# Performance work log

Measured on AMD Instinct MI355X. Metric: run time of the kernel, lower is better.

Reference implementation:

```python
import jax, jax.numpy as jnp
import numpy as np

B, S, D_IN, D_Q, D_V, H = 2, 2048, 1024, 1024, 1024, 16
HD_Q, HD_V = D_Q // H, D_V // H
SCALE = float(D_Q) ** 0.5  # source scales by sqrt(d_q), NOT sqrt(head_dim)


def setup_inputs() -> dict:
    key = jax.random.key(0)
    k1, k2, k3, k4, k5 = jax.random.split(key, 5)
    return {
        "x": jax.random.normal(k1, (B, S, D_IN), dtype=jnp.float32),
        "w_q": jax.random.normal(k2, (D_IN, D_Q), dtype=jnp.float32),
        "w_k": jax.random.normal(k3, (D_IN, D_Q), dtype=jnp.float32),
        "w_v": jax.random.normal(k4, (D_IN, D_V), dtype=jnp.float32),
        "W_o": jax.random.normal(k5, (D_IN, D_V), dtype=jnp.float32),
    }


def reference(x, w_q, w_k, w_v, W_o):
    b, s, _ = x.shape
    # projections: [b, s, d]
    q = x @ w_q
    k = x @ w_k
    v = x @ w_v
    # split heads -> [b, h, s, hd]
    Q = q.reshape(b, s, H, HD_Q).transpose(0, 2, 1, 3)
    K = k.reshape(b, s, H, HD_Q).transpose(0, 2, 1, 3)
    V = v.reshape(b, s, H, HD_V).transpose(0, 2, 1, 3)
    # full [b, h, s, s] score matrix (naive attention, as in source)
    scores = jnp.einsum("bhqd,bhkd->bhqk", Q, K)
    # FAITHFUL QUIRK: source applies softmax over dim=0 (batch axis)
    attn = jax.nn.softmax(scores / SCALE, axis=0)
    vals = jnp.einsum("bhqk,bhkd->bhqd", attn, V)
    vals = vals.transpose(0, 2, 1, 3).reshape(b, s, D_V)
    return vals @ W_o
```

## Files before the change

kernel.cpp:

```cpp
#include <hip/hip_runtime.h>


typedef _Float16 f16;
typedef __attribute__((ext_vector_type(8))) _Float16 f16x8;
typedef __attribute__((ext_vector_type(4))) _Float16 f16x4;
typedef __attribute__((ext_vector_type(4))) float f32x4;

#define MFMA16(a,b,c) __builtin_amdgcn_mfma_f32_16x16x32_f16(a,b,c,0,0,0)
#define GLD16(gp, lp) __builtin_amdgcn_global_load_lds(                         \
    (const __attribute__((address_space(1))) void*)(gp),                        \
    (__attribute__((address_space(3))) void*)(lp), 16, 0, 0)

__global__ __launch_bounds__(256) void convert_x(const float* __restrict__ x,
                                                 f16* __restrict__ xh, int n4) {
    int i = blockIdx.x * 256 + threadIdx.x;
    if (i >= n4) return;
    float4 v = ((const float4*)x)[i];
    f16x4 h;
    h[0] = (f16)v.x; h[1] = (f16)v.y; h[2] = (f16)v.z; h[3] = (f16)v.w;
    *(f16x4*)(xh + (long)i * 4) = h;
}

__global__ __launch_bounds__(256) void transpose_w(const float* __restrict__ w0, const float* __restrict__ w1,
                                                   const float* __restrict__ w2, const float* __restrict__ w3,
                                                   f16* __restrict__ o0, f16* __restrict__ o1,
                                                   f16* __restrict__ o2, f16* __restrict__ o3) {
    const float* w; f16* o;
    switch (blockIdx.z) {
        case 0: w = w0; o = o0; break;
        case 1: w = w1; o = o1; break;
        case 2: w = w2; o = o2; break;
        default: w = w3; o = o3; break;
    }
    __shared__ alignas(16) f16 t[64][72];
    const int tid = threadIdx.x;
    const int d0 = blockIdx.x * 64, j0 = blockIdx.y * 64;
    #pragma unroll
    for (int it = 0; it < 4; ++it) {
        int idx = it * 256 + tid;
        int row = idx >> 4, c4 = idx & 15;
        float4 v = *(const float4*)(w + (long)(d0 + row) * 1024 + j0 + c4 * 4);
        f16x4 h;
        h[0] = (f16)v.x; h[1] = (f16)v.y; h[2] = (f16)v.z; h[3] = (f16)v.w;
        *(f16x4*)&t[row][c4 * 4] = h;
    }
    __syncthreads();
    #pragma unroll
    for (int it = 0; it < 4; ++it) {
        int idx = it * 256 + tid;
        int jr = idx >> 4, d4 = idx & 15;
        f16x4 h;
        #pragma unroll
        for (int m = 0; m < 4; ++m) h[m] = t[d4 * 4 + m][jr];
        *(f16x4*)(o + (long)(j0 + jr) * 1024 + d0 + d4 * 4) = h;
    }
}

__global__ __launch_bounds__(256, 1) void gemm_qkv(const f16* __restrict__ A,
                                                   const f16* __restrict__ Wt,
                                                   f16* __restrict__ Qg,
                                                   f16* __restrict__ Kg,
                                                   f16* __restrict__ Vtg) {
    __shared__ alignas(16) f16 As[128][64];
    __shared__ alignas(16) f16 Bs[128][64];
    const int tid = threadIdx.x;
    const int wave = tid >> 6, lane = tid & 63;
    const int l15 = lane & 15, lq = lane >> 4;
    const int sw = l15 & 7;
    const int m0 = blockIdx.x * 128, n0 = blockIdx.y * 128;
    const int wr = (wave >> 1) * 64, wc = (wave & 1) * 64;
    const int r8 = lane >> 3;
    const int swc8 = ((lane & 7) ^ r8) * 8;

    f32x4 acc[4][4] = {};

    for (int kt = 0; kt < 16; ++kt) {
        __syncthreads();
        #pragma unroll
        for (int i = 0; i < 4; ++i) {
            GLD16(A  + (long)(m0 + wave * 32 + i * 8 + r8) * 1024 + kt * 64 + swc8, &As[wave * 32 + i * 8][0]);
            GLD16(Wt + (long)(n0 + wave * 32 + i * 8 + r8) * 1024 + kt * 64 + swc8, &Bs[wave * 32 + i * 8][0]);
        }
        __syncthreads();
        #pragma unroll
        for (int s2 = 0; s2 < 2; ++s2) {
            const int rc = ((s2 * 4 + lq) ^ sw) << 3;
            f16x8 af[4], bf[4];
            #pragma unroll
            for (int i = 0; i < 4; ++i) af[i] = *(const f16x8*)&As[wr + i * 16 + l15][rc];
            #pragma unroll
            for (int j = 0; j < 4; ++j) bf[j] = *(const f16x8*)&Bs[wc + j * 16 + l15][rc];
            #pragma unroll
            for (int i = 0; i < 4; ++i)
                #pragma unroll
                for (int j = 0; j < 4; ++j)
                    acc[i][j] = MFMA16(af[i], bf[j], acc[i][j]);
        }
    }

    const int sel = n0 >> 10;
    f16* dst = sel == 0 ? Qg : (sel == 1 ? Kg : Vtg);
    const int nb = n0 - (sel << 10);

    #pragma unroll
    for (int i = 0; i < 4; ++i)
        #pragma unroll
        for (int j = 0; j < 4; ++j) {
            int gr0 = m0 + wr + i * 16 + lq * 4;
            int gc  = nb + wc + j * 16 + l15;
            int hh = gc >> 6, hd = gc & 63;
            if (sel == 2) {
                int b = gr0 >> 11, s = gr0 & 2047;
                f16x4 v;
                #pragma unroll
                for (int r = 0; r < 4; ++r) v[r] = (f16)acc[i][j][r];
                *(f16x4*)(dst + (long)((b * 16 + hh) * 64 + hd) * 2048 + s) = v;
            } else {
                #pragma unroll
                for (int r = 0; r < 4; ++r) {
                    int gr = gr0 + r;
                    int b = gr >> 11, s = gr & 2047;
                    dst[(long)((b * 16 + hh) * 2048 + s) * 64 + hd] = (f16)acc[i][j][r];
                }
            }
        }
}

__global__ __launch_bounds__(256, 1) void gemm_out(const f16* __restrict__ A0,
                                                   const f16* __restrict__ A1,
                                                   const f16* __restrict__ Bt,
                                                   float* __restrict__ outp) {
    __shared__ alignas(16) f16 As[64][72];
    __shared__ alignas(16) f16 Bs[128][64];
    const int tid = threadIdx.x;
    const int wave = tid >> 6, lane = tid & 63;
    const int l15 = lane & 15, lq = lane >> 4;
    const int sw = l15 & 7;
    const int m0 = blockIdx.x * 64, n0 = blockIdx.y * 128;
    const int wr = (wave >> 1) * 32, wc = (wave & 1) * 64;
    const int r8 = lane >> 3;
    const int swc8 = ((lane & 7) ^ r8) * 8;

    f32x4 acc[2][4] = {};

    for (int kt = 0; kt < 16; ++kt) {
        __syncthreads();
        #pragma unroll
        for (int it = 0; it < 2; ++it) {
            int idx = it * 256 + tid;
            int row = idx >> 3, c = idx & 7;
            f16x8 a = *(const f16x8*)(A0 + (long)(m0 + row) * 1024 + kt * 64 + c * 8)
                    + *(const f16x8*)(A1 + (long)(m0 + row) * 1024 + kt * 64 + c * 8);
            *(f16x8*)&As[row][c * 8] = a;
        }
        #pragma unroll
        for (int i = 0; i < 4; ++i)
            GLD16(Bt + (long)(n0 + wave * 32 + i * 8 + r8) * 1024 + kt * 64 + swc8, &Bs[wave * 32 + i * 8][0]);
        __syncthreads();
        #pragma unroll
        for (int s2 = 0; s2 < 2; ++s2) {
            const int rc = ((s2 * 4 + lq) ^ sw) << 3;
            f16x8 af[2], bf[4];
            #pragma unroll
            for (int i = 0; i < 2; ++i) af[i] = *(const f16x8*)&As[wr + i * 16 + l15][s2 * 32 + lq * 8];
            #pragma unroll
            for (int j = 0; j < 4; ++j) bf[j] = *(const f16x8*)&Bs[wc + j * 16 + l15][rc];
            #pragma unroll
            for (int i = 0; i < 2; ++i)
                #pragma unroll
                for (int j = 0; j < 4; ++j)
                    acc[i][j] = MFMA16(af[i], bf[j], acc[i][j]);
        }
    }

    #pragma unroll
    for (int i = 0; i < 2; ++i)
        #pragma unroll
        for (int j = 0; j < 4; ++j) {
            int gr0 = m0 + wr + i * 16 + lq * 4;
            int gc  = n0 + wc + j * 16 + l15;
            #pragma unroll
            for (int r = 0; r < 4; ++r)
                outp[(long)(gr0 + r) * 1024 + gc] = acc[i][j][r];
        }
}

__global__ __launch_bounds__(256, 2) void attention_kernel(const f16* __restrict__ Qg,
                                                           const f16* __restrict__ Kg,
                                                           const f16* __restrict__ Vtg,
                                                           f16* __restrict__ vals0,
                                                           f16* __restrict__ vals1) {
    __shared__ alignas(16) f16 Ks [2][64][64];
    __shared__ alignas(16) f16 Vts[2][64][64];
    __shared__ alignas(16) f16 Ps [4][32][64];
    const int tid = threadIdx.x;
    const int wave = tid >> 6, lane = tid & 63;
    const int l15 = lane & 15, lq = lane >> 4;
    const int sw = l15 & 7;

    const int bid = blockIdx.x;
    const int xcd = bid & 7, sl = bid >> 3;
    const int h  = xcd * 2 + (sl & 1);
    const int qt = (sl >> 1) & 15, ks = sl >> 5;
    const int q0 = qt * 128, kt0 = ks * 16;
    f16* vals = ks ? vals1 : vals0;
    const int qr = q0 + wave * 32;

    f16x8 qfr[2][2][2];
    #pragma unroll
    for (int b2 = 0; b2 < 2; ++b2)
        #pragma unroll
        for (int qq = 0; qq < 2; ++qq)
            #pragma unroll
            for (int s2 = 0; s2 < 2; ++s2)
                qfr[b2][qq][s2] = *(const f16x8*)(Qg + (long)((b2 * 16 + h) * 2048 + qr + qq * 16 + l15) * 64
                                                  + s2 * 32 + lq * 8);

    f32x4 acc[2][2][4] = {};

    const int tb = wave & 1;
    const int r8 = lane >> 3;
    const int swc8 = ((lane & 7) ^ r8) * 8;
    const f16* kbase = Kg  + (long)((tb * 16 + h) * 2048 + kt0 * 64) * 64 + r8 * 64 + swc8;
    const f16* vbase = Vtg + (long)((tb * 16 + h) * 64 + r8) * 2048 + kt0 * 64 + swc8;

    for (int kt = 0; kt < 16; ++kt) {
        __syncthreads();
        if (wave < 2) {
            const f16* g = kbase + kt * 4096;
            f16* l = &Ks[tb][0][0];
            #pragma unroll
            for (int i = 0; i < 8; ++i) GLD16(g + i * 512, l + i * 512);
        } else {
            const f16* g = vbase + kt * 64;
            f16* l = &Vts[tb][0][0];
            #pragma unroll
            for (int i = 0; i < 8; ++i) GLD16(g + (long)i * 8 * 2048, l + i * 512);
        }
        __syncthreads();

        f16x4 pp0[2][4], pp1[2][4];
        #pragma unroll
        for (int kf = 0; kf < 4; ++kf) {
            f32x4 S0[2] = {}, S1[2] = {};
            #pragma unroll
            for (int s2 = 0; s2 < 2; ++s2) {
                const int rc = ((s2 * 4 + lq) ^ sw) << 3;
                f16x8 a0 = *(const f16x8*)&Ks[0][kf * 16 + l15][rc];
                f16x8 a1 = *(const f16x8*)&Ks[1][kf * 16 + l15][rc];
                #pragma unroll
                for (int qq = 0; qq < 2; ++qq) {
                    S0[qq] = MFMA16(a0, qfr[0][qq][s2], S0[qq]);
                    S1[qq] = MFMA16(a1, qfr[1][qq][s2], S1[qq]);
                }
            }
            #pragma unroll
            for (int qq = 0; qq < 2; ++qq)
                #pragma unroll
                for (int r = 0; r < 4; ++r) {
                    float d = (S0[qq][r] - S1[qq][r]) * 0.045084219f;
                    float p = __builtin_amdgcn_rcpf(1.0f + __builtin_amdgcn_exp2f(-d));
                    pp0[qq][kf][r] = (f16)p;
                    pp1[qq][kf][r] = (f16)(1.0f - p);
                }
        }

        const int pwsub = (lq & 1) << 2;
        #pragma unroll
        for (int pb = 0; pb < 2; ++pb) {
            #pragma unroll
            for (int qq = 0; qq < 2; ++qq)
                #pragma unroll
                for (int kf = 0; kf < 4; ++kf)
                    *(f16x4*)&Ps[wave][qq * 16 + l15][(((2 * kf + (lq >> 1)) ^ sw) << 3) + pwsub]
                        = pb ? pp1[qq][kf] : pp0[qq][kf];
            #pragma unroll
            for (int s2 = 0; s2 < 2; ++s2) {
                const int rc = ((s2 * 4 + lq) ^ sw) << 3;
                f16x8 pf[2], vf[4];
                #pragma unroll
                for (int qq = 0; qq < 2; ++qq)
                    pf[qq] = *(const f16x8*)&Ps[wave][qq * 16 + l15][rc];
                #pragma unroll
                for (int hf = 0; hf < 4; ++hf)
                    vf[hf] = *(const f16x8*)&Vts[pb][hf * 16 + l15][rc];
                #pragma unroll
                for (int qq = 0; qq < 2; ++qq)
                    #pragma unroll
                    for (int hf = 0; hf < 4; ++hf)
                        acc[pb][qq][hf] = MFMA16(pf[qq], vf[hf], acc[pb][qq][hf]);
            }
        }
    }

    #pragma unroll
    for (int b2 = 0; b2 < 2; ++b2)
        #pragma unroll
        for (int qq = 0; qq < 2; ++qq)
            #pragma unroll
            for (int hf = 0; hf < 4; ++hf)
                #pragma unroll
                for (int r = 0; r < 4; ++r)
                    vals[(long)(b2 * 2048 + qr + qq * 16 + lq * 4 + r) * 1024 + h * 64 + hf * 16 + l15]
                        = (f16)acc[b2][qq][hf][r];
}

extern "C" void kernel_launch(void* const* d_in, const int* in_sizes, int n_in,
                              void* d_out, int out_size, void* d_ws, size_t ws_size,
                              hipStream_t stream) {
    const float* x  = (const float*)d_in[0];
    const float* wq = (const float*)d_in[1];
    const float* wk = (const float*)d_in[2];
    const float* wv = (const float*)d_in[3];
    const float* wo = (const float*)d_in[4];

    char* ws = (char*)d_ws;
    f16* xh    = (f16*)(ws);
    f16* wqT   = (f16*)(ws + 8388608);
    f16* wkT   = (f16*)(ws + 10485760);
    f16* wvT   = (f16*)(ws + 12582912);
    f16* woT   = (f16*)(ws + 14680064);
    f16* Qg    = (f16*)(ws + 16777216);
    f16* Kg    = (f16*)(ws + 25165824);
    f16* Vtg   = (f16*)(ws + 33554432);
    f16* vals1 = (f16*)(ws + 41943040);
    f16* vals0 = xh;
    (void)ws_size; (void)in_sizes; (void)n_in; (void)out_size;

    convert_x<<<4096, 256, 0, stream>>>(x, xh, (2 * 2048 * 1024) / 4);
    transpose_w<<<dim3(16, 16, 4), 256, 0, stream>>>(wq, wk, wv, wo, wqT, wkT, wvT, woT);

    gemm_qkv<<<dim3(32, 24), 256, 0, stream>>>(xh, wqT, Qg, Kg, Vtg);

    attention_kernel<<<512, 256, 0, stream>>>(Qg, Kg, Vtg, vals0, vals1);

    gemm_out<<<dim3(64, 8), 256, 0, stream>>>(vals0, vals1, woT, (float*)d_out);
}
```

Baseline: 194.6 us.

## Stage Q/K epilogue through LDS for vector stores, fold scale, shrink attention blocks

The QKV GEMM epilogue for Q and K now goes through a swizzled LDS tile, so each head row is written to global memory with 16-byte vector stores instead of scattered 2-byte stores. The softmax scale (with the log2e factor) is folded into Q at write time, which removes a multiply per score in attention. Attention blocks drop from 4 waves to 2 and cover 64 query rows, and the grid doubles to 1024 blocks. Each block therefore loads both batches' K/V tiles with fewer waves, trading per-block load parallelism and K/V reuse for more blocks in flight.

```diff
diff --git a/kernel.cpp b/kernel.cpp
--- a/kernel.cpp
+++ b/kernel.cpp
@@ -61,8 +61,9 @@
                                                    f16* __restrict__ Qg,
                                                    f16* __restrict__ Kg,
                                                    f16* __restrict__ Vtg) {
-    __shared__ alignas(16) f16 As[128][64];
-    __shared__ alignas(16) f16 Bs[128][64];
+    __shared__ alignas(16) f16 smem[16384];
+    f16* As = smem;
+    f16* Bs = smem + 8192;
     const int tid = threadIdx.x;
     const int wave = tid >> 6, lane = tid & 63;
     const int l15 = lane & 15, lq = lane >> 4;
@@ -78,8 +79,8 @@
         __syncthreads();
         #pragma unroll
         for (int i = 0; i < 4; ++i) {
-            GLD16(A  + (long)(m0 + wave * 32 + i * 8 + r8) * 1024 + kt * 64 + swc8, &As[wave * 32 + i * 8][0]);
-            GLD16(Wt + (long)(n0 + wave * 32 + i * 8 + r8) * 1024 + kt * 64 + swc8, &Bs[wave * 32 + i * 8][0]);
+            GLD16(A  + (long)(m0 + wave * 32 + i * 8 + r8) * 1024 + kt * 64 + swc8, As + (wave * 32 + i * 8) * 64);
+            GLD16(Wt + (long)(n0 + wave * 32 + i * 8 + r8) * 1024 + kt * 64 + swc8, Bs + (wave * 32 + i * 8) * 64);
         }
         __syncthreads();
         #pragma unroll
@@ -87,9 +88,9 @@
             const int rc = ((s2 * 4 + lq) ^ sw) << 3;
             f16x8 af[4], bf[4];
             #pragma unroll
-            for (int i = 0; i < 4; ++i) af[i] = *(const f16x8*)&As[wr + i * 16 + l15][rc];
-            #pragma unroll
-            for (int j = 0; j < 4; ++j) bf[j] = *(const f16x8*)&Bs[wc + j * 16 + l15][rc];
+            for (int i = 0; i < 4; ++i) af[i] = *(const f16x8*)&As[(wr + i * 16 + l15) * 64 + rc];
+            #pragma unroll
+            for (int j = 0; j < 4; ++j) bf[j] = *(const f16x8*)&Bs[(wc + j * 16 + l15) * 64 + rc];
             #pragma unroll
             for (int i = 0; i < 4; ++i)
                 #pragma unroll
@@ -99,31 +100,50 @@
     }
 
     const int sel = n0 >> 10;
-    f16* dst = sel == 0 ? Qg : (sel == 1 ? Kg : Vtg);
     const int nb = n0 - (sel << 10);
 
-    #pragma unroll
-    for (int i = 0; i < 4; ++i)
-        #pragma unroll
-        for (int j = 0; j < 4; ++j) {
-            int gr0 = m0 + wr + i * 16 + lq * 4;
-            int gc  = nb + wc + j * 16 + l15;
-            int hh = gc >> 6, hd = gc & 63;
-            if (sel == 2) {
-                int b = gr0 >> 11, s = gr0 & 2047;
-                f16x4 v;
-                #pragma unroll
-                for (int r = 0; r < 4; ++r) v[r] = (f16)acc[i][j][r];
-                *(f16x4*)(dst + (long)((b * 16 + hh) * 64 + hd) * 2048 + s) = v;
-            } else {
+    if (sel < 2) {
+        f16* dst = sel == 0 ? Qg : Kg;
+        const float qs = sel == 0 ? 0.045084219f : 1.0f;
+        __syncthreads();
+        #pragma unroll
+        for (int i = 0; i < 4; ++i)
+            #pragma unroll
+            for (int j = 0; j < 4; ++j) {
+                int row0 = wr + i * 16 + lq * 4;
+                int colb = wc + j * 16 + l15;
+                int chunk = colb >> 3, sub = colb & 7;
                 #pragma unroll
                 for (int r = 0; r < 4; ++r) {
-                    int gr = gr0 + r;
-                    int b = gr >> 11, s = gr & 2047;
-                    dst[(long)((b * 16 + hh) * 2048 + s) * 64 + hd] = (f16)acc[i][j][r];
+                    int row = row0 + r;
+                    smem[row * 128 + ((chunk ^ (row & 7)) << 3) + sub] = (f16)(acc[i][j][r] * qs);
                 }
             }
-        }
+        __syncthreads();
+        #pragma unroll
+        for (int e = 0; e < 8; ++e) {
+            int id = e * 256 + tid;
+            int row = id >> 4, c = id & 15;
+            f16x8 v = *(const f16x8*)&smem[row * 128 + ((c ^ (row & 7)) << 3)];
+            int gr = m0 + row, b = gr >> 11, s = gr & 2047;
+            int gc = nb + c * 8, hh = gc >> 6, hd = gc & 63;
+            *(f16x8*)(dst + (long)((b * 16 + hh) * 2048 + s) * 64 + hd) = v;
+        }
+    } else {
+        #pragma unroll
+        for (int i = 0; i < 4; ++i)
+            #pragma unroll
+            for (int j = 0; j < 4; ++j) {
+                int gr0 = m0 + wr + i * 16 + lq * 4;
+                int gc  = nb + wc + j * 16 + l15;
+                int b = gr0 >> 11, s = gr0 & 2047;
+                int hh = gc >> 6, hd = gc & 63;
+                f16x4 v;
+                #pragma unroll
+                for (int r = 0; r < 4; ++r) v[r] = (f16)acc[i][j][r];
+                *(f16x4*)(Vtg + (long)((b * 16 + hh) * 64 + hd) * 2048 + s) = v;
+            }
+    }
 }
 
 __global__ __launch_bounds__(256, 1) void gemm_out(const f16* __restrict__ A0,
@@ -185,14 +205,14 @@
         }
 }
 
-__global__ __launch_bounds__(256, 2) void attention_kernel(const f16* __restrict__ Qg,
+__global__ __launch_bounds__(128, 2) void attention_kernel(const f16* __restrict__ Qg,
                                                            const f16* __restrict__ Kg,
                                                            const f16* __restrict__ Vtg,
                                                            f16* __restrict__ vals0,
                                                            f16* __restrict__ vals1) {
     __shared__ alignas(16) f16 Ks [2][64][64];
     __shared__ alignas(16) f16 Vts[2][64][64];
-    __shared__ alignas(16) f16 Ps [4][32][64];
+    __shared__ alignas(16) f16 Ps [2][32][64];
     const int tid = threadIdx.x;
     const int wave = tid >> 6, lane = tid & 63;
     const int l15 = lane & 15, lq = lane >> 4;
@@ -201,8 +221,8 @@
     const int bid = blockIdx.x;
     const int xcd = bid & 7, sl = bid >> 3;
     const int h  = xcd * 2 + (sl & 1);
-    const int qt = (sl >> 1) & 15, ks = sl >> 5;
-    const int q0 = qt * 128, kt0 = ks * 16;
+    const int qt = (sl >> 1) & 31, ks = sl >> 6;
+    const int q0 = qt * 64, kt0 = ks * 16;
     f16* vals = ks ? vals1 : vals0;
     const int qr = q0 + wave * 32;
 
@@ -218,24 +238,29 @@
 
     f32x4 acc[2][2][4] = {};
 
-    const int tb = wave & 1;
     const int r8 = lane >> 3;
     const int swc8 = ((lane & 7) ^ r8) * 8;
-    const f16* kbase = Kg  + (long)((tb * 16 + h) * 2048 + kt0 * 64) * 64 + r8 * 64 + swc8;
-    const f16* vbase = Vtg + (long)((tb * 16 + h) * 64 + r8) * 2048 + kt0 * 64 + swc8;
+    const f16* kb0 = Kg  + (long)(h * 2048 + kt0 * 64) * 64 + r8 * 64 + swc8;
+    const f16* kb1 = kb0 + (long)16 * 2048 * 64;
+    const f16* vb0 = Vtg + (long)(h * 64 + r8) * 2048 + kt0 * 64 + swc8;
+    const f16* vb1 = vb0 + (long)16 * 64 * 2048;
 
     for (int kt = 0; kt < 16; ++kt) {
         __syncthreads();
-        if (wave < 2) {
-            const f16* g = kbase + kt * 4096;
-            f16* l = &Ks[tb][0][0];
-            #pragma unroll
-            for (int i = 0; i < 8; ++i) GLD16(g + i * 512, l + i * 512);
+        if (wave == 0) {
+            const f16* g0 = kb0 + kt * 4096;
+            const f16* g1 = kb1 + kt * 4096;
+            #pragma unroll
+            for (int i = 0; i < 8; ++i) GLD16(g0 + i * 512, &Ks[0][0][0] + i * 512);
+            #pragma unroll
+            for (int i = 0; i < 8; ++i) GLD16(g1 + i * 512, &Ks[1][0][0] + i * 512);
         } else {
-            const f16* g = vbase + kt * 64;
-            f16* l = &Vts[tb][0][0];
-            #pragma unroll
-            for (int i = 0; i < 8; ++i) GLD16(g + (long)i * 8 * 2048, l + i * 512);
+            const f16* g0 = vb0 + kt * 64;
+            const f16* g1 = vb1 + kt * 64;
+            #pragma unroll
+            for (int i = 0; i < 8; ++i) GLD16(g0 + (long)i * 8 * 2048, &Vts[0][0][0] + i * 512);
+            #pragma unroll
+            for (int i = 0; i < 8; ++i) GLD16(g1 + (long)i * 8 * 2048, &Vts[1][0][0] + i * 512);
         }
         __syncthreads();
 
@@ -258,8 +283,8 @@
             for (int qq = 0; qq < 2; ++qq)
                 #pragma unroll
                 for (int r = 0; r < 4; ++r) {
-                    float d = (S0[qq][r] - S1[qq][r]) * 0.045084219f;
-                    float p = __builtin_amdgcn_rcpf(1.0f + __builtin_amdgcn_exp2f(-d));
+                    float e = __builtin_amdgcn_exp2f(S1[qq][r] - S0[qq][r]);
+                    float p = __builtin_amdgcn_rcpf(1.0f + e);
                     pp0[qq][kf][r] = (f16)p;
                     pp1[qq][kf][r] = (f16)(1.0f - p);
                 }
@@ -332,7 +357,7 @@
 
     gemm_qkv<<<dim3(32, 24), 256, 0, stream>>>(xh, wqT, Qg, Kg, Vtg);
 
-    attention_kernel<<<512, 256, 0, stream>>>(Qg, Kg, Vtg, vals0, vals1);
+    attention_kernel<<<1024, 128, 0, stream>>>(Qg, Kg, Vtg, vals0, vals1);
 
     gemm_out<<<dim3(64, 8), 256, 0, stream>>>(vals0, vals1, woT, (float*)d_out);
 }
```

Result: no change. 195.8 us (+0.6%).
